# Kernel optimization log

Hardware: AMD Instinct MI355X
Metric: run time of the kernel (lower is better)

The kernel has to match this reference:

```python
import jax, jax.numpy as jnp
import numpy as np

B, H, W, WS = 8, 64, 64, 8
C = CY = 512
NH = 16
HD = C // NH
N = WS * WS
MLP_H = 4 * C

def _rel_pos_index(ws):
    coords = np.stack(np.meshgrid(np.arange(ws), np.arange(ws), indexing='ij')).reshape(2, -1)
    rel = (coords[:, :, None] - coords[:, None, :]).transpose(1, 2, 0)
    rel[:, :, 0] += ws - 1
    rel[:, :, 1] += ws - 1
    rel[:, :, 0] *= 2 * ws - 1
    return jnp.asarray(rel.sum(-1))  # (N, N) int

REL_IDX = _rel_pos_index(WS)

def _ln(x, g, b, eps=1e-4):
    m = x.mean(-1, keepdims=True)
    v = ((x - m) ** 2).mean(-1, keepdims=True)
    return (x - m) * jax.lax.rsqrt(v + eps) * g + b

def _win_part(x):
    b, h, w, c = x.shape
    return x.reshape(b, h // WS, WS, w // WS, WS, c).transpose(0, 1, 3, 2, 4, 5).reshape(-1, WS * WS, c)

def _win_rev(xw, b, h, w):
    c = xw.shape[-1]
    return xw.reshape(b, h // WS, w // WS, WS, WS, c).transpose(0, 1, 3, 2, 4, 5).reshape(b, h, w, c)

def _mlp(x, w1, bb1, w2, bb2):
    return jax.nn.gelu(x @ w1 + bb1, approximate=False) @ w2 + bb2

def _block(x, y, nuclei_mask, rpb_table, g1, b1, g3, b3, w_qkv, b_qkv, w_qkv_y, b_qkv_y, w_qx, b_qx, w_qy, b_qy, w_proj, b_proj, w_proj_y, b_proj_y, g2, b2, g4, b4, w_fc1, b_fc1, w_fc2, b_fc2, w_fc1y, b_fc1y, w_fc2y, b_fc2y):
    Bn, L, _ = x.shape
    sx, sy = x, y
    xw = _win_part(_ln(x, g1, b1).reshape(Bn, H, W, C))       # (B_, N, C)
    yw = _win_part(_ln(y, g3, b3).reshape(Bn, H, W, CY))      # (B_, N, CY)
    nm = _win_part(nuclei_mask.reshape(Bn, H, W, 1))[..., 0]  # (B_, N)
    kv = (xw @ w_qkv + b_qkv).reshape(-1, N, 2, NH, HD).transpose(2, 0, 3, 1, 4)
    k, v = kv[0], kv[1]
    kvy = (yw @ w_qkv_y + b_qkv_y).reshape(-1, N, 2, NH, HD).transpose(2, 0, 3, 1, 4)
    k_y, v_y = kvy[0], kvy[1]
    scale = HD ** -0.5
    q = (xw @ w_qx + b_qx).reshape(-1, N, NH, HD).transpose(0, 2, 1, 3) * scale    # x-queries attend y
    q_y = (yw @ w_qy + b_qy).reshape(-1, N, NH, HD).transpose(0, 2, 1, 3) * scale  # y-queries attend x
    bias = rpb_table[REL_IDX].transpose(2, 0, 1)[None]  # (1, NH, N, N) relative position bias
    # nuclei mask fusion: the torch permute/cat chain is exactly attn[q,k] += m[q] + m[k]
    m = nm[:, None, :, None] + nm[:, None, None, :]     # (B_, 1, N, N)
    attn_x = jax.nn.softmax(jnp.einsum('bhqd,bhkd->bhqk', q_y, k) + bias + m, axis=-1)
    attn_y = jax.nn.softmax(jnp.einsum('bhqd,bhkd->bhqk', q, k_y) + bias + m, axis=-1)
    ox = jnp.einsum('bhqk,bhkd->bhqd', attn_x, v).transpose(0, 2, 1, 3).reshape(-1, N, C) @ w_proj + b_proj
    oy = jnp.einsum('bhqk,bhkd->bhqd', attn_y, v_y).transpose(0, 2, 1, 3).reshape(-1, N, CY) @ w_proj_y + b_proj_y
    x = sx + _win_rev(ox, Bn, H, W).reshape(Bn, L, C)
    y = sy + _win_rev(oy, Bn, H, W).reshape(Bn, L, CY)
    x = x + _mlp(_ln(x, g2, b2), w_fc1, b_fc1, w_fc2, b_fc2)
    y = y + _mlp(_ln(y, g4, b4), w_fc1y, b_fc1y, w_fc2y, b_fc2y)
    return x, y

def setup_inputs() -> dict:
    key = jax.random.key(0)
    ks = iter(jax.random.split(key, 48))
    def nrm(shape, s=0.02):
        return jax.random.normal(next(ks), shape, jnp.float32) * s
    inp = {
        'x': jax.random.normal(next(ks), (B, H * W, C), jnp.float32),
        'y': jax.random.normal(next(ks), (B, H * W, CY), jnp.float32),
        'nuclei_mask': jax.random.normal(next(ks), (B, H * W, 1), jnp.float32),
        'rpb_table': nrm(((2 * WS - 1) ** 2, NH)),
        'g1': jnp.ones((C,), jnp.float32), 'b1': jnp.zeros((C,), jnp.float32),
        'g3': jnp.ones((CY,), jnp.float32), 'b3': jnp.zeros((CY,), jnp.float32),
        'w_qkv': nrm((C, 2 * C)), 'b_qkv': jnp.zeros((2 * C,), jnp.float32),
        'w_qkv_y': nrm((CY, 2 * CY)), 'b_qkv_y': jnp.zeros((2 * CY,), jnp.float32),
        'w_qx': nrm((C, CY)), 'b_qx': jnp.zeros((CY,), jnp.float32),
        'w_qy': nrm((CY, C)), 'b_qy': jnp.zeros((C,), jnp.float32),
        'w_proj': nrm((C, C)), 'b_proj': jnp.zeros((C,), jnp.float32),
        'w_proj_y': nrm((CY, CY)), 'b_proj_y': jnp.zeros((CY,), jnp.float32),
        'g2': jnp.ones((C,), jnp.float32), 'b2': jnp.zeros((C,), jnp.float32),
        'g4': jnp.ones((CY,), jnp.float32), 'b4': jnp.zeros((CY,), jnp.float32),
        'w_fc1': nrm((C, MLP_H)), 'b_fc1': jnp.zeros((MLP_H,), jnp.float32),
        'w_fc2': nrm((MLP_H, C)), 'b_fc2': jnp.zeros((C,), jnp.float32),
        'w_fc1y': nrm((CY, MLP_H)), 'b_fc1y': jnp.zeros((MLP_H,), jnp.float32),
        'w_fc2y': nrm((MLP_H, CY)), 'b_fc2y': jnp.zeros((CY,), jnp.float32),
    }
    return inp

def reference(x, y, nuclei_mask, rpb_table, g1, b1, g3, b3, w_qkv, b_qkv, w_qkv_y, b_qkv_y, w_qx, b_qx, w_qy, b_qy, w_proj, b_proj, w_proj_y, b_proj_y, g2, b2, g4, b4, w_fc1, b_fc1, w_fc2, b_fc2, w_fc1y, b_fc1y, w_fc2y, b_fc2y):
    return _block(x, y, nuclei_mask, rpb_table, g1, b1, g3, b3, w_qkv, b_qkv, w_qkv_y, b_qkv_y, w_qx, b_qx, w_qy, b_qy, w_proj, b_proj, w_proj_y, b_proj_y, g2, b2, g4, b4, w_fc1, b_fc1, w_fc2, b_fc2, w_fc1y, b_fc1y, w_fc2y, b_fc2y)
```

## Files before the change

### kernel.cpp

```cpp
#include <hip/hip_runtime.h>


typedef __attribute__((ext_vector_type(8))) short bf16x8;
typedef __attribute__((ext_vector_type(4))) float f32x4;

#define NTOK 32768
#define CDIM 512

__device__ __forceinline__ unsigned short f2bf(float f) {
  unsigned int u = __float_as_uint(f);
  u = (u + 0x7fffu + ((u >> 16) & 1u)) >> 16;
  return (unsigned short)u;
}
__device__ __forceinline__ float bf2f(unsigned short u) {
  return __uint_as_float(((unsigned int)u) << 16);
}

__device__ __forceinline__ void gload_lds16(const void* g, void* l) {
  __builtin_amdgcn_global_load_lds(
      (const __attribute__((address_space(1))) void*)g,
      (__attribute__((address_space(3))) void*)l, 16, 0, 0);
}

struct TpArgs { const float* W[4]; unsigned short* O[4]; };

__global__ __launch_bounds__(256)
void transpose_w(TpArgs ta, int K, int N) {
  __shared__ float tile[64][65];
  const float* __restrict__ W = ta.W[blockIdx.z];
  unsigned short* __restrict__ Wt = ta.O[blockIdx.z];
  const int n0 = blockIdx.x * 64, k0 = blockIdx.y * 64;
  const int c = threadIdx.x & 63, rb = threadIdx.x >> 6;
#pragma unroll
  for (int i = 0; i < 16; ++i) {
    int r = i * 4 + rb;
    tile[r][c] = W[(long)(k0 + r) * N + n0 + c];
  }
  __syncthreads();
#pragma unroll
  for (int i = 0; i < 16; ++i) {
    int rn = i * 4 + rb;
    Wt[(long)(n0 + rn) * K + k0 + c] = f2bf(tile[c][rn]);
  }
}

__global__ __launch_bounds__(256)
void pack_bias(const float* bkv0, const float* bq0,
               const float* bkv1, const float* bq1,
               float* o0, float* o1) {
  const int i = blockIdx.x * 256 + threadIdx.x;
  o0[i] = (i < 1024) ? bkv0[i] : bq0[i - 1024];
  o1[i] = (i < 1024) ? bkv1[i] : bq1[i - 1024];
}

__global__ __launch_bounds__(256)
void ln_f32(const float* X0, const float* X1,
            const float* g0_, const float* b0_,
            const float* g1_, const float* b1_,
            unsigned short* o0, unsigned short* o1) {
  const int zz = blockIdx.y;
  const float* __restrict__ X = zz ? X1 : X0;
  const float* __restrict__ g = zz ? g1_ : g0_;
  const float* __restrict__ b = zz ? b1_ : b0_;
  unsigned short* __restrict__ out = zz ? o1 : o0;

  const int lane = threadIdx.x & 63;
  const int wid = threadIdx.x >> 6;
  const long t = (long)blockIdx.x * 4 + wid;
  const float* x = X + t * CDIM + lane * 8;
  float4 v0 = *(const float4*)x;
  float4 v1 = *(const float4*)(x + 4);
  float s = v0.x + v0.y + v0.z + v0.w + v1.x + v1.y + v1.z + v1.w;
  float sq = v0.x * v0.x + v0.y * v0.y + v0.z * v0.z + v0.w * v0.w +
             v1.x * v1.x + v1.y * v1.y + v1.z * v1.z + v1.w * v1.w;
#pragma unroll
  for (int off = 32; off; off >>= 1) {
    s += __shfl_xor(s, off);
    sq += __shfl_xor(sq, off);
  }
  const float mean = s * (1.0f / 512.0f);
  const float var = sq * (1.0f / 512.0f) - mean * mean;
  const float rs = rsqrtf(var + 1e-4f);
  float4 g0 = *(const float4*)(g + lane * 8);
  float4 g1 = *(const float4*)(g + lane * 8 + 4);
  float4 b0 = *(const float4*)(b + lane * 8);
  float4 b1 = *(const float4*)(b + lane * 8 + 4);
  bf16x8 r;
  r[0] = (short)f2bf((v0.x - mean) * rs * g0.x + b0.x);
  r[1] = (short)f2bf((v0.y - mean) * rs * g0.y + b0.y);
  r[2] = (short)f2bf((v0.z - mean) * rs * g0.z + b0.z);
  r[3] = (short)f2bf((v0.w - mean) * rs * g0.w + b0.w);
  r[4] = (short)f2bf((v1.x - mean) * rs * g1.x + b1.x);
  r[5] = (short)f2bf((v1.y - mean) * rs * g1.y + b1.y);
  r[6] = (short)f2bf((v1.z - mean) * rs * g1.z + b1.z);
  r[7] = (short)f2bf((v1.w - mean) * rs * g1.w + b1.w);
  *(bf16x8*)(out + t * CDIM + lane * 8) = r;
}

__global__ __launch_bounds__(256)
void ln_b16(const unsigned short* X0, const unsigned short* X1,
            const float* g0_, const float* b0_,
            const float* g1_, const float* b1_,
            unsigned short* o0, unsigned short* o1) {
  const int zz = blockIdx.y;
  const unsigned short* __restrict__ X = zz ? X1 : X0;
  const float* __restrict__ g = zz ? g1_ : g0_;
  const float* __restrict__ b = zz ? b1_ : b0_;
  unsigned short* __restrict__ out = zz ? o1 : o0;

  const int lane = threadIdx.x & 63;
  const int wid = threadIdx.x >> 6;
  const long t = (long)blockIdx.x * 4 + wid;
  bf16x8 v = *(const bf16x8*)(X + t * CDIM + lane * 8);
  float f[8];
  float s = 0.f, sq = 0.f;
#pragma unroll
  for (int i = 0; i < 8; ++i) {
    f[i] = bf2f((unsigned short)v[i]);
    s += f[i]; sq += f[i] * f[i];
  }
#pragma unroll
  for (int off = 32; off; off >>= 1) {
    s += __shfl_xor(s, off);
    sq += __shfl_xor(sq, off);
  }
  const float mean = s * (1.0f / 512.0f);
  const float var = sq * (1.0f / 512.0f) - mean * mean;
  const float rs = rsqrtf(var + 1e-4f);
  float4 g0 = *(const float4*)(g + lane * 8);
  float4 g1 = *(const float4*)(g + lane * 8 + 4);
  float4 b0 = *(const float4*)(b + lane * 8);
  float4 b1 = *(const float4*)(b + lane * 8 + 4);
  const float gg[8] = {g0.x, g0.y, g0.z, g0.w, g1.x, g1.y, g1.z, g1.w};
  const float bb[8] = {b0.x, b0.y, b0.z, b0.w, b1.x, b1.y, b1.z, b1.w};
  bf16x8 r;
#pragma unroll
  for (int i = 0; i < 8; ++i)
    r[i] = (short)f2bf((f[i] - mean) * rs * gg[i] + bb[i]);
  *(bf16x8*)(out + t * CDIM + lane * 8) = r;
}


struct PairArgs {
  const unsigned short* A0; const unsigned short* A1;
  const unsigned short* B0; const unsigned short* B1;
  const float* bias0; const float* bias1;
  const void* r0; const void* r1;
  void* o0; void* o1;
};

template <int EPI>
__global__ __launch_bounds__(512, 4)
void gemm_mt(PairArgs pa, float scale, int M, int N, int K) {
  __shared__ __attribute__((aligned(16))) char lds[81920];

  const int z = blockIdx.z;
  const unsigned short* __restrict__ A  = z ? pa.A1 : pa.A0;
  const unsigned short* __restrict__ Bt = z ? pa.B1 : pa.B0;
  const float* __restrict__ bias = z ? pa.bias1 : pa.bias0;
  const void* resid = z ? pa.r1 : pa.r0;
  void* outp = z ? pa.o1 : pa.o0;

  const int nwg = gridDim.x * gridDim.y;
  int wg = blockIdx.y * gridDim.x + blockIdx.x;
  {
    const int q8 = nwg >> 3, r8 = nwg & 7;
    const int xcd = wg & 7, o = wg >> 3;
    wg = (xcd < r8 ? xcd * (q8 + 1) : r8 * (q8 + 1) + (xcd - r8) * q8) + o;
  }
  const int bx = wg % gridDim.x, by = wg / gridDim.x;

  const int tid = threadIdx.x;
  const int lane = tid & 63;
  const int wid = tid >> 6;
  const int wr = wid >> 1;
  const int wc = wid & 1;
  const long rowBase = (long)by * 256;
  const long colBase = (long)bx * 128;

  const unsigned short* Ap = A + rowBase * K;
  const unsigned short* Bp = Bt + colBase * K;

  const int srow = tid >> 3;
  const int sslot = (tid & 7) ^ (srow & 7);

  auto stA = [&](int buf, int k0, int i) {
    gload_lds16(Ap + (long)(i * 64 + srow) * K + k0 + sslot * 8,
                lds + buf * 32768 + i * 8192 + tid * 16);
  };
  auto stB = [&](int k0, int i) {
    gload_lds16(Bp + (long)(i * 64 + srow) * K + k0 + sslot * 8,
                lds + 65536 + i * 8192 + tid * 16);
  };

  const int lo = lane & 15;
  const int hi = lane >> 4;
  const int x7 = lane & 7;
  const int arow0 = (wr * 64 + lo) * 128;
  const int brow0 = 65536 + (wc * 64 + lo) * 128;

  f32x4 acc[4][4] = {};

  const int nt = K / 64;

  stA(0, 0, 0); stA(0, 0, 1); stA(0, 0, 2); stA(0, 0, 3);

  for (int t = 0; t < nt; ++t) {
    const int cur = t & 1;
    const int k0 = t * 64;
    const bool pf = (t + 1 < nt);

    stB(k0, 0); stB(k0, 1);
    if (pf) {
      const int k1 = k0 + 64;
      stA(cur ^ 1, k1, 0); stA(cur ^ 1, k1, 1);
      stA(cur ^ 1, k1, 2); stA(cur ^ 1, k1, 3);
      asm volatile("s_waitcnt vmcnt(4)" ::: "memory");
    } else {
      asm volatile("s_waitcnt vmcnt(0)" ::: "memory");
    }
    __builtin_amdgcn_sched_barrier(0);
    __builtin_amdgcn_s_barrier();

#pragma unroll
    for (int kk = 0; kk < 2; ++kk) {
      const int cb = ((kk * 4 + hi) ^ x7) * 16;
      bf16x8 af[4], bf[4];
#pragma unroll
      for (int m = 0; m < 4; ++m)
        af[m] = *(const bf16x8*)(lds + cur * 32768 + arow0 + m * 2048 + cb);
#pragma unroll
      for (int n = 0; n < 4; ++n)
        bf[n] = *(const bf16x8*)(lds + brow0 + n * 2048 + cb);
#pragma unroll
      for (int m = 0; m < 4; ++m)
#pragma unroll
        for (int n = 0; n < 4; ++n)
          acc[m][n] = __builtin_amdgcn_mfma_f32_16x16x32_bf16(af[m], bf[n], acc[m][n], 0, 0, 0);
    }
    if (pf) __builtin_amdgcn_s_barrier();
  }

#pragma unroll
  for (int m = 0; m < 4; ++m) {
    const long rbase = rowBase + wr * 64 + m * 16 + hi * 4;
#pragma unroll
    for (int n = 0; n < 4; ++n) {
      const long col = colBase + wc * 64 + n * 16 + lo;
      const float bv = bias[col];
#pragma unroll
      for (int r = 0; r < 4; ++r) {
        float v = acc[m][n][r] + bv;
        if constexpr (EPI == 2) {
          const float tt = 1.5957691216057308f * v * (1.0f + 0.044715f * v * v);
          v = v * __fdividef(1.0f, 1.0f + __expf(-tt));
        }
        if constexpr (EPI == 4) { if (col >= 1024) v *= scale; }
        const long idx = (rbase + r) * (long)N + col;
        if constexpr (EPI == 5) {
          ((unsigned short*)outp)[idx] = f2bf(v + ((const float*)resid)[idx]);
        } else if constexpr (EPI == 6) {
          ((float*)outp)[idx] = v + bf2f(((const unsigned short*)resid)[idx]);
        } else {
          ((unsigned short*)outp)[idx] = f2bf(v);
        }
      }
    }
  }
}

__global__ __launch_bounds__(256)
void attn_win(const unsigned short* __restrict__ qx_,
              const unsigned short* __restrict__ kvx_,
              unsigned short* __restrict__ ox_,
              const unsigned short* __restrict__ qy_,
              const unsigned short* __restrict__ kvy_,
              unsigned short* __restrict__ oy_,
              const float* __restrict__ nmask,
              const float* __restrict__ rpb) {
  __shared__ float nm_s[64];
  __shared__ unsigned short rpb_s[3600];
  __shared__ unsigned short P_s[4][64][72];
  __shared__ unsigned short Vt_s[4][32][72];

  const unsigned short* qbuf; const unsigned short* kvbuf; unsigned short* obuf;
  if (blockIdx.y == 0) { qbuf = qy_; kvbuf = kvx_; obuf = ox_; }
  else                 { qbuf = qx_; kvbuf = kvy_; obuf = oy_; }

  const int tid = threadIdx.x;
  const int lane = tid & 63;
  const int wid = tid >> 6;
  const int wi = blockIdx.x;
  const int wbase = (wi >> 6) * 4096 + ((wi >> 3) & 7) * 512 + (wi & 7) * 8;

  if (tid < 64) nm_s[tid] = nmask[wbase + ((tid >> 3) << 6) + (tid & 7)];
  for (int i = tid; i < 3600; i += 256) rpb_s[i] = f2bf(rpb[i]);
  __syncthreads();

  const int r0 = (lane >> 4) * 4;
  const int cn = lane & 15;
  const int kb8 = (lane >> 4) * 8;

  for (int hh = 0; hh < 4; ++hh) {
    const int h = wid * 4 + hh;

    f32x4 s[4][4] = {};
    {
      bf16x8 qa[4], kb[4];
#pragma unroll
      for (int m = 0; m < 4; ++m) {
        const int r = m * 16 + cn;
        const long tok = wbase + ((r >> 3) << 6) + (r & 7);
        qa[m] = *(const bf16x8*)(qbuf + tok * 1536 + h * 32 + kb8);
      }
#pragma unroll
      for (int n = 0; n < 4; ++n) {
        const int c = n * 16 + cn;
        const long tok = wbase + ((c >> 3) << 6) + (c & 7);
        kb[n] = *(const bf16x8*)(kvbuf + tok * 1536 + h * 32 + kb8);
      }
#pragma unroll
      for (int m = 0; m < 4; ++m)
#pragma unroll
        for (int n = 0; n < 4; ++n)
          s[m][n] = __builtin_amdgcn_mfma_f32_16x16x32_bf16(qa[m], kb[n], s[m][n], 0, 0, 0);
    }

#pragma unroll
    for (int m = 0; m < 4; ++m) {
#pragma unroll
      for (int r = 0; r < 4; ++r) {
        const int q = m * 16 + r0 + r;
        const int qi = q >> 3, qj = q & 7;
        float rowv[4];
#pragma unroll
        for (int n = 0; n < 4; ++n) {
          const int k = n * 16 + cn;
          const int ki = k >> 3, kj = k & 7;
          const int ridx = (qi - ki + 7) * 15 + (qj - kj + 7);
          rowv[n] = s[m][n][r] + bf2f(rpb_s[ridx * 16 + h]) + nm_s[q] + nm_s[k];
        }
        float mx = fmaxf(fmaxf(rowv[0], rowv[1]), fmaxf(rowv[2], rowv[3]));
#pragma unroll
        for (int off = 8; off; off >>= 1) mx = fmaxf(mx, __shfl_xor(mx, off));
        float sum = 0.f;
#pragma unroll
        for (int n = 0; n < 4; ++n) { rowv[n] = __expf(rowv[n] - mx); sum += rowv[n]; }
#pragma unroll
        for (int off = 8; off; off >>= 1) sum += __shfl_xor(sum, off);
        const float inv = 1.0f / sum;
#pragma unroll
        for (int n = 0; n < 4; ++n) s[m][n][r] = rowv[n] * inv;
      }
    }

#pragma unroll
    for (int m = 0; m < 4; ++m)
#pragma unroll
      for (int n = 0; n < 4; ++n)
#pragma unroll
        for (int r = 0; r < 4; ++r)
          P_s[wid][m * 16 + r0 + r][n * 16 + cn] = f2bf(s[m][n][r]);

    {
      const long tok = wbase + ((lane >> 3) << 6) + (lane & 7);
      const unsigned short* vrow = kvbuf + tok * 1536 + 512 + h * 32;
#pragma unroll
      for (int j = 0; j < 4; ++j) {
        bf16x8 vv = *(const bf16x8*)(vrow + j * 8);
#pragma unroll
        for (int e = 0; e < 8; ++e)
          Vt_s[wid][j * 8 + e][lane] = (unsigned short)vv[e];
      }
    }

    f32x4 o[4][2] = {};
#pragma unroll
    for (int t = 0; t < 2; ++t) {
      bf16x8 paf[4], vb[2];
#pragma unroll
      for (int m = 0; m < 4; ++m)
        paf[m] = *(const bf16x8*)(&P_s[wid][m * 16 + cn][t * 32 + kb8]);
#pragma unroll
      for (int n = 0; n < 2; ++n)
        vb[n] = *(const bf16x8*)(&Vt_s[wid][n * 16 + cn][t * 32 + kb8]);
#pragma unroll
      for (int m = 0; m < 4; ++m)
#pragma unroll
        for (int n = 0; n < 2; ++n)
          o[m][n] = __builtin_amdgcn_mfma_f32_16x16x32_bf16(paf[m], vb[n], o[m][n], 0, 0, 0);
    }

#pragma unroll
    for (int m = 0; m < 4; ++m) {
#pragma unroll
      for (int r = 0; r < 4; ++r) {
        const int q = m * 16 + r0 + r;
        const long tok = wbase + ((q >> 3) << 6) + (q & 7);
#pragma unroll
        for (int n = 0; n < 2; ++n)
          obuf[tok * 512 + h * 32 + n * 16 + cn] = f2bf(o[m][n][r]);
      }
    }
  }
}

extern "C" void kernel_launch(void* const* d_in, const int* in_sizes, int n_in,
                              void* d_out, int out_size, void* d_ws, size_t ws_size,
                              hipStream_t stream) {
  const float* x = (const float*)d_in[0];
  const float* y = (const float*)d_in[1];
  const float* nmk = (const float*)d_in[2];
  const float* rpb = (const float*)d_in[3];
  const float* g1 = (const float*)d_in[4];
  const float* b1 = (const float*)d_in[5];
  const float* g3 = (const float*)d_in[6];
  const float* b3 = (const float*)d_in[7];
  const float* w_qkv = (const float*)d_in[8];
  const float* b_qkv = (const float*)d_in[9];
  const float* w_qkv_y = (const float*)d_in[10];
  const float* b_qkv_y = (const float*)d_in[11];
  const float* w_qx = (const float*)d_in[12];
  const float* b_qx = (const float*)d_in[13];
  const float* w_qy = (const float*)d_in[14];
  const float* b_qy = (const float*)d_in[15];
  const float* w_proj = (const float*)d_in[16];
  const float* b_proj = (const float*)d_in[17];
  const float* w_proj_y = (const float*)d_in[18];
  const float* b_proj_y = (const float*)d_in[19];
  const float* g2 = (const float*)d_in[20];
  const float* b2 = (const float*)d_in[21];
  const float* g4 = (const float*)d_in[22];
  const float* b4 = (const float*)d_in[23];
  const float* w_fc1 = (const float*)d_in[24];
  const float* b_fc1 = (const float*)d_in[25];
  const float* w_fc2 = (const float*)d_in[26];
  const float* b_fc2 = (const float*)d_in[27];
  const float* w_fc1y = (const float*)d_in[28];
  const float* b_fc1y = (const float*)d_in[29];
  const float* w_fc2y = (const float*)d_in[30];
  const float* b_fc2y = (const float*)d_in[31];

  char* ws = (char*)d_ws;
  unsigned short* wT_kvq_x = (unsigned short*)(ws + 0);
  unsigned short* wT_kvq_y = (unsigned short*)(ws + 1572864);
  unsigned short* w_projT  = (unsigned short*)(ws + 3145728);
  unsigned short* w_projyT = (unsigned short*)(ws + 3670016);
  unsigned short* w_fc1T   = (unsigned short*)(ws + 4194304);
  unsigned short* w_fc2T   = (unsigned short*)(ws + 6291456);
  unsigned short* w_fc1yT  = (unsigned short*)(ws + 8388608);
  unsigned short* w_fc2yT  = (unsigned short*)(ws + 10485760);
  float* bias_kvq_x = (float*)(ws + 12582912);
  float* bias_kvq_y = (float*)(ws + 12589056);
  unsigned short* XLN  = (unsigned short*)(ws + 79704064);
  unsigned short* YLN  = (unsigned short*)(ws + 113258496);
  unsigned short* KVQX = (unsigned short*)(ws + 146812928);
  unsigned short* KVQY = (unsigned short*)(ws + 247476224);
  unsigned short* X1   = (unsigned short*)(ws + 348139520);
  unsigned short* Y1   = (unsigned short*)(ws + 381693952);
  unsigned short* X2LN   = KVQX;
  unsigned short* Y2LN   = (unsigned short*)(ws + 180367360);
  unsigned short* HBUF_X = (unsigned short*)(ws + 12595200);
  unsigned short* HBUF_Y = (unsigned short*)(ws + 213921792);

  float* out_x = (float*)d_out;
  float* out_y = out_x + 16777216;

  {
    TpArgs ta{{w_qkv, w_qkv_y, nullptr, nullptr},
              {wT_kvq_x, wT_kvq_y, nullptr, nullptr}};
    transpose_w<<<dim3(16, 8, 2), 256, 0, stream>>>(ta, 512, 1024);
  }
  {
    TpArgs ta{{w_qx, w_qy, w_proj, w_proj_y},
              {wT_kvq_x + 1024 * 512, wT_kvq_y + 1024 * 512, w_projT, w_projyT}};
    transpose_w<<<dim3(8, 8, 4), 256, 0, stream>>>(ta, 512, 512);
  }
  {
    TpArgs ta{{w_fc1, w_fc1y, nullptr, nullptr}, {w_fc1T, w_fc1yT, nullptr, nullptr}};
    transpose_w<<<dim3(32, 8, 2), 256, 0, stream>>>(ta, 512, 2048);
  }
  {
    TpArgs ta{{w_fc2, w_fc2y, nullptr, nullptr}, {w_fc2T, w_fc2yT, nullptr, nullptr}};
    transpose_w<<<dim3(8, 32, 2), 256, 0, stream>>>(ta, 2048, 512);
  }

  pack_bias<<<6, 256, 0, stream>>>(b_qkv, b_qx, b_qkv_y, b_qy,
                                   bias_kvq_x, bias_kvq_y);

  ln_f32<<<dim3(8192, 2), 256, 0, stream>>>(x, y, g1, b1, g3, b3, XLN, YLN);

  const float qscale = 0.17677669529663687f;
  {
    PairArgs pa{XLN, YLN, wT_kvq_x, wT_kvq_y, bias_kvq_x, bias_kvq_y,
                nullptr, nullptr, KVQX, KVQY};
    gemm_mt<4><<<dim3(12, 128, 2), 512, 0, stream>>>(pa, qscale, NTOK, 1536, 512);
  }

  attn_win<<<dim3(512, 2), 256, 0, stream>>>(KVQX + 1024, KVQX, XLN,
                                             KVQY + 1024, KVQY, YLN, nmk, rpb);

  {
    PairArgs pa{XLN, YLN, w_projT, w_projyT, b_proj, b_proj_y, x, y, X1, Y1};
    gemm_mt<5><<<dim3(4, 128, 2), 512, 0, stream>>>(pa, 1.f, NTOK, 512, 512);
  }

  ln_b16<<<dim3(8192, 2), 256, 0, stream>>>(X1, Y1, g2, b2, g4, b4, X2LN, Y2LN);

  {
    PairArgs pa{X2LN, Y2LN, w_fc1T, w_fc1yT, b_fc1, b_fc1y,
                nullptr, nullptr, HBUF_X, HBUF_Y};
    gemm_mt<2><<<dim3(16, 128, 2), 512, 0, stream>>>(pa, 1.f, NTOK, 2048, 512);
  }
  {
    PairArgs pa{HBUF_X, HBUF_Y, w_fc2T, w_fc2yT, b_fc2, b_fc2y,
                X1, Y1, out_x, out_y};
    gemm_mt<6><<<dim3(4, 128, 2), 512, 0, stream>>>(pa, 1.f, NTOK, 512, 2048);
  }
}
```

Baseline: 752.6 us.

## Shrink GEMM K-tile to 32 with double-buffered A and B in LDS

The GEMM main loop moves from a 64-wide K tile (double-buffered A, single-buffered B, 80KB LDS) to a 32-wide K tile with both A and B double-buffered in 48KB LDS. The XOR swizzle is changed to match the 64-byte row stride. The smaller LDS footprint is meant to let more workgroups fit per CU and to hide B-load latency by prefetching B as well. In exchange there are twice as many loop iterations and barriers, each doing half the MFMA work.

```diff
diff --git a/kernel.cpp b/kernel.cpp
--- a/kernel.cpp
+++ b/kernel.cpp
@@ -152,7 +152,7 @@
 template <int EPI>
 __global__ __launch_bounds__(512, 4)
 void gemm_mt(PairArgs pa, float scale, int M, int N, int K) {
-  __shared__ __attribute__((aligned(16))) char lds[81920];
+  __shared__ __attribute__((aligned(16))) char lds[49152];
 
   const int z = blockIdx.z;
   const unsigned short* __restrict__ A  = z ? pa.A1 : pa.A0;
@@ -181,57 +181,54 @@
   const unsigned short* Ap = A + rowBase * K;
   const unsigned short* Bp = Bt + colBase * K;
 
-  const int srow = tid >> 3;
-  const int sslot = (tid & 7) ^ (srow & 7);
+  const int srow = tid >> 2;
+  const int scol = ((tid & 3) ^ ((srow >> 1) & 3)) * 8;
 
   auto stA = [&](int buf, int k0, int i) {
-    gload_lds16(Ap + (long)(i * 64 + srow) * K + k0 + sslot * 8,
-                lds + buf * 32768 + i * 8192 + tid * 16);
+    gload_lds16(Ap + (long)(i * 128 + srow) * K + k0 + scol,
+                lds + buf * 16384 + i * 8192 + tid * 16);
   };
-  auto stB = [&](int k0, int i) {
-    gload_lds16(Bp + (long)(i * 64 + srow) * K + k0 + sslot * 8,
-                lds + 65536 + i * 8192 + tid * 16);
+  auto stB = [&](int buf, int k0) {
+    gload_lds16(Bp + (long)srow * K + k0 + scol,
+                lds + 32768 + buf * 8192 + tid * 16);
   };
 
   const int lo = lane & 15;
   const int hi = lane >> 4;
-  const int x7 = lane & 7;
-  const int arow0 = (wr * 64 + lo) * 128;
-  const int brow0 = 65536 + (wc * 64 + lo) * 128;
+  const int cb = (hi ^ ((lo >> 1) & 3)) * 16;
+  const int arow0 = (wr * 64 + lo) * 64;
+  const int brow0 = (wc * 64 + lo) * 64;
 
   f32x4 acc[4][4] = {};
 
-  const int nt = K / 64;
-
-  stA(0, 0, 0); stA(0, 0, 1); stA(0, 0, 2); stA(0, 0, 3);
+  const int nt = K / 32;
+
+  stA(0, 0, 0); stA(0, 0, 1); stB(0, 0);
 
   for (int t = 0; t < nt; ++t) {
     const int cur = t & 1;
-    const int k0 = t * 64;
+    const int abase = cur * 16384;
+    const int bbase = 32768 + cur * 8192;
     const bool pf = (t + 1 < nt);
 
-    stB(k0, 0); stB(k0, 1);
     if (pf) {
-      const int k1 = k0 + 64;
-      stA(cur ^ 1, k1, 0); stA(cur ^ 1, k1, 1);
-      stA(cur ^ 1, k1, 2); stA(cur ^ 1, k1, 3);
-      asm volatile("s_waitcnt vmcnt(4)" ::: "memory");
+      const int k1 = (t + 1) * 32;
+      stA(cur ^ 1, k1, 0); stA(cur ^ 1, k1, 1); stB(cur ^ 1, k1);
+      asm volatile("s_waitcnt vmcnt(3)" ::: "memory");
     } else {
       asm volatile("s_waitcnt vmcnt(0)" ::: "memory");
     }
     __builtin_amdgcn_sched_barrier(0);
     __builtin_amdgcn_s_barrier();
 
-#pragma unroll
-    for (int kk = 0; kk < 2; ++kk) {
-      const int cb = ((kk * 4 + hi) ^ x7) * 16;
+    {
       bf16x8 af[4], bf[4];
 #pragma unroll
       for (int m = 0; m < 4; ++m)
-        af[m] = *(const bf16x8*)(lds + cur * 32768 + arow0 + m * 2048 + cb);
+        af[m] = *(const bf16x8*)(lds + abase + arow0 + m * 1024 + cb);
 #pragma unroll
       for (int n = 0; n < 4; ++n)
-        bf[n] = *(const bf16x8*)(lds + brow0 + n * 2048 + cb);
+        bf[n] = *(const bf16x8*)(lds + bbase + brow0 + n * 1024 + cb);
 #pragma unroll
       for (int m = 0; m < 4; ++m)
 #pragma unroll
```

After: 806.1 us. 1.07x slower.

## Run MLP fc2 GEMM in FP8 e4m3 with fp8 hidden activations

Applied to the files above, without the earlier changes.

The fc1 epilogue now writes its GELU output as FP8 e4m3 instead of bf16, and the fc2 weights are transposed into FP8. A new gemm_f8 kernel uses fp8 MFMA with a 128-byte K step. This halves hidden-buffer traffic and uses the higher-throughput fp8 matrix path for the largest GEMM, in exchange for reduced precision in activations and weights that may exceed the accuracy tolerance.

```diff
diff --git a/kernel.cpp b/kernel.cpp
--- a/kernel.cpp
+++ b/kernel.cpp
@@ -14,6 +14,25 @@
 }
 __device__ __forceinline__ float bf2f(unsigned short u) {
   return __uint_as_float(((unsigned int)u) << 16);
+}
+
+__device__ __forceinline__ unsigned char f2e4m3(float f) {
+  unsigned int u = __float_as_uint(f);
+  unsigned char s = (unsigned char)((u >> 24) & 0x80u);
+  unsigned int m = u & 0x7fffffffu;
+  if (m >= 0x43E80000u) return s | 0x7Eu;
+  if (m < 0x3C800000u) {
+    float d = __uint_as_float(m) * 512.0f;
+    int di = __float2int_rn(d);
+    if (di >= 8) return s | 0x08u;
+    return s | (unsigned char)di;
+  }
+  unsigned int q = m + 0x0007FFFFu + ((m >> 20) & 1u);
+  q >>= 20;
+  int v = (int)q - ((127 - 7) << 3);
+  if (v <= 0) return s;
+  if (v > 0x7E) v = 0x7E;
+  return s | (unsigned char)v;
 }
 
 __device__ __forceinline__ void gload_lds16(const void* g, void* l) {
@@ -41,6 +60,28 @@
   for (int i = 0; i < 16; ++i) {
     int rn = i * 4 + rb;
     Wt[(long)(n0 + rn) * K + k0 + c] = f2bf(tile[c][rn]);
+  }
+}
+
+struct Tp8Args { const float* W[2]; unsigned char* O[2]; };
+
+__global__ __launch_bounds__(256)
+void transpose_w8(Tp8Args ta, int K, int N) {
+  __shared__ float tile[64][65];
+  const float* __restrict__ W = ta.W[blockIdx.z];
+  unsigned char* __restrict__ Wt = ta.O[blockIdx.z];
+  const int n0 = blockIdx.x * 64, k0 = blockIdx.y * 64;
+  const int c = threadIdx.x & 63, rb = threadIdx.x >> 6;
+#pragma unroll
+  for (int i = 0; i < 16; ++i) {
+    int r = i * 4 + rb;
+    tile[r][c] = W[(long)(k0 + r) * N + n0 + c];
+  }
+  __syncthreads();
+#pragma unroll
+  for (int i = 0; i < 16; ++i) {
+    int rn = i * 4 + rb;
+    Wt[(long)(n0 + rn) * K + k0 + c] = f2e4m3(tile[c][rn]);
   }
 }
 
@@ -142,8 +183,8 @@
 
 
 struct PairArgs {
-  const unsigned short* A0; const unsigned short* A1;
-  const unsigned short* B0; const unsigned short* B1;
+  const void* A0; const void* A1;
+  const void* B0; const void* B1;
   const float* bias0; const float* bias1;
   const void* r0; const void* r1;
   void* o0; void* o1;
@@ -155,8 +196,8 @@
   __shared__ __attribute__((aligned(16))) char lds[81920];
 
   const int z = blockIdx.z;
-  const unsigned short* __restrict__ A  = z ? pa.A1 : pa.A0;
-  const unsigned short* __restrict__ Bt = z ? pa.B1 : pa.B0;
+  const unsigned short* __restrict__ A  = (const unsigned short*)(z ? pa.A1 : pa.A0);
+  const unsigned short* __restrict__ Bt = (const unsigned short*)(z ? pa.B1 : pa.B0);
   const float* __restrict__ bias = z ? pa.bias1 : pa.bias0;
   const void* resid = z ? pa.r1 : pa.r0;
   void* outp = z ? pa.o1 : pa.o0;
@@ -251,19 +292,126 @@
 #pragma unroll
       for (int r = 0; r < 4; ++r) {
         float v = acc[m][n][r] + bv;
+        const long idx = (rbase + r) * (long)N + col;
         if constexpr (EPI == 2) {
           const float tt = 1.5957691216057308f * v * (1.0f + 0.044715f * v * v);
           v = v * __fdividef(1.0f, 1.0f + __expf(-tt));
-        }
-        if constexpr (EPI == 4) { if (col >= 1024) v *= scale; }
-        const long idx = (rbase + r) * (long)N + col;
-        if constexpr (EPI == 5) {
+          ((unsigned char*)outp)[idx] = f2e4m3(v);
+        } else if constexpr (EPI == 4) {
+          if (col >= 1024) v *= scale;
+          ((unsigned short*)outp)[idx] = f2bf(v);
+        } else if constexpr (EPI == 5) {
           ((unsigned short*)outp)[idx] = f2bf(v + ((const float*)resid)[idx]);
-        } else if constexpr (EPI == 6) {
-          ((float*)outp)[idx] = v + bf2f(((const unsigned short*)resid)[idx]);
         } else {
           ((unsigned short*)outp)[idx] = f2bf(v);
         }
+      }
+    }
+  }
+}
+
+__global__ __launch_bounds__(512, 4)
+void gemm_f8(PairArgs pa, int M, int N, int K) {
+  __shared__ __attribute__((aligned(16))) char lds[81920];
+
+  const int z = blockIdx.z;
+  const unsigned char* __restrict__ A  = (const unsigned char*)(z ? pa.A1 : pa.A0);
+  const unsigned char* __restrict__ Bt = (const unsigned char*)(z ? pa.B1 : pa.B0);
+  const float* __restrict__ bias = z ? pa.bias1 : pa.bias0;
+  const unsigned short* __restrict__ resid =
+      (const unsigned short*)(z ? pa.r1 : pa.r0);
+  float* __restrict__ outp = (float*)(z ? pa.o1 : pa.o0);
+
+  const int nwg = gridDim.x * gridDim.y;
+  int wg = blockIdx.y * gridDim.x + blockIdx.x;
+  {
+    const int q8 = nwg >> 3, r8 = nwg & 7;
+    const int xcd = wg & 7, o = wg >> 3;
+    wg = (xcd < r8 ? xcd * (q8 + 1) : r8 * (q8 + 1) + (xcd - r8) * q8) + o;
+  }
+  const int bx = wg % gridDim.x, by = wg / gridDim.x;
+
+  const int tid = threadIdx.x;
+  const int lane = tid & 63;
+  const int wid = tid >> 6;
+  const int wr = wid >> 1;
+  const int wc = wid & 1;
+  const long rowBase = (long)by * 256;
+  const long colBase = (long)bx * 128;
+
+  const unsigned char* Ap = A + rowBase * K;
+  const unsigned char* Bp = Bt + colBase * K;
+
+  const int srow = tid >> 3;
+  const int schunk = ((tid & 7) ^ (srow & 7)) * 16;
+
+  auto stA = [&](int buf, int k0, int i) {
+    gload_lds16(Ap + (long)(i * 64 + srow) * K + k0 + schunk,
+                lds + buf * 32768 + i * 8192 + tid * 16);
+  };
+  auto stB = [&](int k0, int i) {
+    gload_lds16(Bp + (long)(i * 64 + srow) * K + k0 + schunk,
+                lds + 65536 + i * 8192 + tid * 16);
+  };
+
+  const int lo = lane & 15;
+  const int hi = lane >> 4;
+  const int arow0 = (wr * 64 + lo) * 128;
+  const int brow0 = 65536 + (wc * 64 + lo) * 128;
+
+  f32x4 acc[4][4] = {};
+
+  const int nt = K / 128;
+
+  stA(0, 0, 0); stA(0, 0, 1); stA(0, 0, 2); stA(0, 0, 3);
+
+  for (int t = 0; t < nt; ++t) {
+    const int cur = t & 1;
+    const int k0 = t * 128;
+    const bool pf = (t + 1 < nt);
+
+    stB(k0, 0); stB(k0, 1);
+    if (pf) {
+      const int k1 = k0 + 128;
+      stA(cur ^ 1, k1, 0); stA(cur ^ 1, k1, 1);
+      stA(cur ^ 1, k1, 2); stA(cur ^ 1, k1, 3);
+      asm volatile("s_waitcnt vmcnt(4)" ::: "memory");
+    } else {
+      asm volatile("s_waitcnt vmcnt(0)" ::: "memory");
+    }
+    __builtin_amdgcn_sched_barrier(0);
+    __builtin_amdgcn_s_barrier();
+
+#pragma unroll
+    for (int kk = 0; kk < 4; ++kk) {
+      const int cb = (((kk * 2 + (hi >> 1)) ^ (lo & 7)) * 16) + (hi & 1) * 8;
+      long af[4], bq[4];
+#pragma unroll
+      for (int m = 0; m < 4; ++m)
+        af[m] = *(const long*)(lds + cur * 32768 + arow0 + m * 2048 + cb);
+#pragma unroll
+      for (int n = 0; n < 4; ++n)
+        bq[n] = *(const long*)(lds + brow0 + n * 2048 + cb);
+#pragma unroll
+      for (int m = 0; m < 4; ++m)
+#pragma unroll
+        for (int n = 0; n < 4; ++n)
+          acc[m][n] = __builtin_amdgcn_mfma_f32_16x16x32_fp8_fp8(af[m], bq[n], acc[m][n], 0, 0, 0);
+    }
+    if (pf) __builtin_amdgcn_s_barrier();
+  }
+
+#pragma unroll
+  for (int m = 0; m < 4; ++m) {
+    const long rbase = rowBase + wr * 64 + m * 16 + hi * 4;
+#pragma unroll
+    for (int n = 0; n < 4; ++n) {
+      const long col = colBase + wc * 64 + n * 16 + lo;
+      const float bv = bias[col];
+#pragma unroll
+      for (int r = 0; r < 4; ++r) {
+        const long idx = (rbase + r) * (long)N + col;
+        outp[idx] = acc[m][n][r] + bv + bf2f(resid[idx]);
       }
     }
   }
@@ -447,9 +595,9 @@
   unsigned short* w_projT  = (unsigned short*)(ws + 3145728);
   unsigned short* w_projyT = (unsigned short*)(ws + 3670016);
   unsigned short* w_fc1T   = (unsigned short*)(ws + 4194304);
-  unsigned short* w_fc2T   = (unsigned short*)(ws + 6291456);
+  unsigned char*  w_fc2T8  = (unsigned char*)(ws + 6291456);
   unsigned short* w_fc1yT  = (unsigned short*)(ws + 8388608);
-  unsigned short* w_fc2yT  = (unsigned short*)(ws + 10485760);
+  unsigned char*  w_fc2yT8 = (unsigned char*)(ws + 10485760);
   float* bias_kvq_x = (float*)(ws + 12582912);
   float* bias_kvq_y = (float*)(ws + 12589056);
   unsigned short* XLN  = (unsigned short*)(ws + 79704064);
@@ -460,8 +608,8 @@
   unsigned short* Y1   = (unsigned short*)(ws + 381693952);
   unsigned short* X2LN   = KVQX;
   unsigned short* Y2LN   = (unsigned short*)(ws + 180367360);
-  unsigned short* HBUF_X = (unsigned short*)(ws + 12595200);
-  unsigned short* HBUF_Y = (unsigned short*)(ws + 213921792);
+  unsigned char*  HBUF_X8 = (unsigned char*)(ws + 12595200);
+  unsigned char*  HBUF_Y8 = (unsigned char*)(ws + 213921792);
 
   float* out_x = (float*)d_out;
   float* out_y = out_x + 16777216;
@@ -481,8 +629,8 @@
     transpose_w<<<dim3(32, 8, 2), 256, 0, stream>>>(ta, 512, 2048);
   }
   {
-    TpArgs ta{{w_fc2, w_fc2y, nullptr, nullptr}, {w_fc2T, w_fc2yT, nullptr, nullptr}};
-    transpose_w<<<dim3(8, 32, 2), 256, 0, stream>>>(ta, 2048, 512);
+    Tp8Args ta{{w_fc2, w_fc2y}, {w_fc2T8, w_fc2yT8}};
+    transpose_w8<<<dim3(8, 32, 2), 256, 0, stream>>>(ta, 2048, 512);
   }
 
   pack_bias<<<6, 256, 0, stream>>>(b_qkv, b_qx, b_qkv_y, b_qy,
@@ -509,12 +657,12 @@
 
   {
     PairArgs pa{X2LN, Y2LN, w_fc1T, w_fc1yT, b_fc1, b_fc1y,
-                nullptr, nullptr, HBUF_X, HBUF_Y};
+                nullptr, nullptr, HBUF_X8, HBUF_Y8};
     gemm_mt<2><<<dim3(16, 128, 2), 512, 0, stream>>>(pa, 1.f, NTOK, 2048, 512);
   }
   {
-    PairArgs pa{HBUF_X, HBUF_Y, w_fc2T, w_fc2yT, b_fc2, b_fc2y,
+    PairArgs pa{HBUF_X8, HBUF_Y8, w_fc2T8, w_fc2yT8, b_fc2, b_fc2y,
                 X1, Y1, out_x, out_y};
-    gemm_mt<6><<<dim3(4, 128, 2), 512, 0, stream>>>(pa, 1.f, NTOK, 512, 2048);
-  }
-}
+    gemm_f8<<<dim3(4, 128, 2), 512, 0, stream>>>(pa, NTOK, 512, 2048);
+  }
+}
```

Measured after the change: 761.3 us. Within noise of the previous version (+1.2%).
